# Performance work log

Hardware: AMD Instinct MI355X
Metric: run time of the kernel (lower is better)

## Reference

```python
import jax, jax.numpy as jnp
import numpy as np

B, S, K, D, H, F = 2, 2048, 2048, 1024, 16, 4096
HD = D // H
LN_EPS = 1e-5  # nn.LayerNorm default (module's eps arg is unused by the norms)


def setup_inputs() -> dict:
    key = jax.random.key(0)
    ks = jax.random.split(key, 12)
    def w(k, shape, scale=0.02):
        return jax.random.normal(k, shape, jnp.float32) * scale
    return {
        "x": jax.random.normal(ks[0], (B, S, D), jnp.float32),
        "context": jax.random.normal(ks[1], (B, K, D), jnp.float32),
        "Wq": w(ks[2], (D, D)), "bq": jnp.zeros((D,), jnp.float32),
        "Wk": w(ks[3], (D, D)), "bk": jnp.zeros((D,), jnp.float32),
        "Wv": w(ks[4], (D, D)), "bv": jnp.zeros((D,), jnp.float32),
        "W1": w(ks[5], (F, D)), "b1": jnp.zeros((F,), jnp.float32),
        "W2": w(ks[6], (D, F)), "b2": jnp.zeros((D,), jnp.float32),
        "g1": jnp.ones((D,), jnp.float32), "be1": jnp.zeros((D,), jnp.float32),
        "g2": jnp.ones((D,), jnp.float32), "be2": jnp.zeros((D,), jnp.float32),
    }


def _ln(x, g, b):
    m = jnp.mean(x, axis=-1, keepdims=True)
    v = jnp.var(x, axis=-1, keepdims=True)
    return (x - m) / jnp.sqrt(v + LN_EPS) * g + b


def _split_heads(t, L):
    # [B, L, D] -> [B, H, L, HD]
    return t.reshape(B, L, H, HD).transpose(0, 2, 1, 3)


def reference(x, context, Wq, bq, Wk, bk, Wv, bv, W1, b1, W2, b2, g1, be1, g2, be2):
    q = _split_heads(x @ Wq.T + bq, S)
    k = _split_heads(context @ Wk.T + bk, K)
    v = _split_heads(context @ Wv.T + bv, K)
    # NOTE: original scales by sqrt(encoder_out_dim), not sqrt(head_dim)
    scores = jnp.einsum('bhqd,bhkd->bhqk', q, k) / jnp.sqrt(jnp.float32(D))
    attn = jax.nn.softmax(scores, axis=-1)
    ctx = jnp.einsum('bhqk,bhkd->bhqd', attn, v)
    # faithful to original: raw reshape of [B,H,S,HD] -> [B,S,D] (no head transpose)
    out1 = ctx.reshape(B, S, D)
    out1 = x + _ln(out1, g1, be1)
    h = jax.nn.gelu(out1 @ W1.T + b1, approximate=False)
    out2 = _ln(h @ W2.T + b2, g2, be2)
    return out1 + out2
```

## Files before the change

### kernel.cpp

```cpp
#include <hip/hip_runtime.h>
#include <hip/hip_bf16.h>

#define BB 2
#define SS 2048
#define KK 2048
#define DD 1024
#define HH 16
#define FF 4096

using bf16x8 = __attribute__((ext_vector_type(8))) __bf16;
using f32x4  = __attribute__((ext_vector_type(4))) float;
using u16 = unsigned short;

__device__ __forceinline__ float bf2f(u16 u){
  union { unsigned int i; float f; } c; c.i = ((unsigned int)u) << 16; return c.f;
}
__device__ __forceinline__ u16 f2bf(float f){
  union { float f; unsigned int i; } c; c.f = f;
  return (u16)((c.i + 0x7fffu + ((c.i >> 16) & 1u)) >> 16);
}
__device__ __forceinline__ float gelu_exact(float x){
  return 0.5f * x * (1.f + erff(x * 0.70710678118654752f));
}

__device__ __forceinline__ void gll16(const void* g, const void* l) {
  __builtin_amdgcn_global_load_lds(
      (const __attribute__((address_space(1))) void*)(unsigned long long)(size_t)g,
      (__attribute__((address_space(3))) void*)(unsigned int)(size_t)l,
      16, 0, 0);
}

#define E_X   0
#define E_CX  4194304
#define E_WQ  8388608
#define E_BQ  9437184
#define E_WK  9438208
#define E_BK  10486784
#define E_WV  10487808
#define E_BV  11536384
#define E_W1  11537408
#define E_B1  15731712
#define E_W2  15735808
#define E_B2  19930112
#define E_G1  19931136
#define E_BE1 19932160
#define E_G2  19933184
#define E_BE2 19934208
#define E_TOT 19935232

struct Ptrs { const void* p[16]; };

__global__ __launch_bounds__(256)
void convert_inputs(Ptrs ptrs, u16* __restrict__ dst)
{
  const bool is_f32 = (((const u16*)ptrs.p[12])[0] == 0);
  const int szs[16] = {4194304, 4194304, 1048576, 1024, 1048576, 1024,
                       1048576, 1024, 4194304, 4096, 4194304, 1024,
                       1024, 1024, 1024, 1024};
  long long gbase = (long long)blockIdx.x * 1024;
  int seg = 0; long long start = 0;
  while (seg < 15 && gbase >= start + szs[seg]) { start += szs[seg]; seg++; }
  const long long local = gbase - start;
  const int tid = threadIdx.x;
  u16 outv[4];
  if (is_f32) {
    const float4* s = (const float4*)((const float*)ptrs.p[seg] + local);
    float4 v = s[tid];
    outv[0] = f2bf(v.x); outv[1] = f2bf(v.y); outv[2] = f2bf(v.z); outv[3] = f2bf(v.w);
  } else {
    const uint2* s = (const uint2*)((const u16*)ptrs.p[seg] + local);
    uint2 v = s[tid];
    *(uint2*)outv = v;
  }
  *(uint2*)(dst + gbase + (long long)tid * 4) = *(uint2*)outv;
}

template<int EPI>
__device__ __forceinline__
void gemm_core(const u16* __restrict__ A, const u16* __restrict__ W,
               const u16* __restrict__ bias, void* __restrict__ Cout,
               int N, int Kd, int lda, int n0, int m0,
               u16* sA0, u16* sA1, u16* sB0, u16* sB1)
{
  const int tid = threadIdx.x;
  const int wv = tid >> 6, lane = tid & 63;
  const int wm = (wv >> 1) * 64, wn = (wv & 1) * 64;
  const int l16 = lane & 15, quad = lane >> 4;
  const int srow = tid >> 2;
  const int scol = ((tid & 3) ^ ((srow >> 1) & 3)) * 8;

  const u16* gA = A + (size_t)(m0 + srow) * lda + scol;
  const u16* gB = W + (size_t)(n0 + srow) * lda + scol;
  u16* lA0 = sA0 + wv * 512; u16* lA1 = sA1 + wv * 512;
  u16* lB0 = sB0 + wv * 512; u16* lB1 = sB1 + wv * 512;
  const size_t rs = (size_t)64 * lda;

  f32x4 acc[4][4] = {};

  auto mma_step = [&](const u16* sA, const u16* sB) {
    bf16x8 af[4], wf[4];
#pragma unroll
    for (int i = 0; i < 4; i++) {
      const int row = wm + 16 * i + l16;
      af[i] = *(const bf16x8*)(sA + row * 32 + (quad ^ ((row >> 1) & 3)) * 8);
    }
#pragma unroll
    for (int j = 0; j < 4; j++) {
      const int row = wn + 16 * j + l16;
      wf[j] = *(const bf16x8*)(sB + row * 32 + (quad ^ ((row >> 1) & 3)) * 8);
    }
#pragma unroll
    for (int i = 0; i < 4; i++)
#pragma unroll
      for (int j = 0; j < 4; j++)
        acc[i][j] = __builtin_amdgcn_mfma_f32_16x16x32_bf16(af[i], wf[j], acc[i][j], 0, 0, 0);
  };

  gll16(gA, lA0); gll16(gA + rs, lA0 + 2048);
  gll16(gB, lB0); gll16(gB + rs, lB0 + 2048);

  for (int k0 = 0; k0 < Kd; k0 += 64) {
    __syncthreads();
    gll16(gA + k0 + 32, lA1); gll16(gA + rs + k0 + 32, lA1 + 2048);
    gll16(gB + k0 + 32, lB1); gll16(gB + rs + k0 + 32, lB1 + 2048);
    mma_step(sA0, sB0);
    __syncthreads();
    if (k0 + 64 < Kd) {
      gll16(gA + k0 + 64, lA0); gll16(gA + rs + k0 + 64, lA0 + 2048);
      gll16(gB + k0 + 64, lB0); gll16(gB + rs + k0 + 64, lB0 + 2048);
    }
    mma_step(sA1, sB1);
  }

#pragma unroll
  for (int i = 0; i < 4; i++)
#pragma unroll
    for (int j = 0; j < 4; j++) {
      const int mb = m0 + wm + 16 * i + quad * 4;
      const int n  = n0 + wn + 16 * j + l16;
      if (EPI == 4) {
#pragma unroll
        for (int r = 0; r < 4; r++)
          ((float*)Cout)[(size_t)(mb + r) * N + n] = acc[i][j][r];
      } else {
        const float bv = bf2f(bias[n]);
        if (EPI == 3) {
          u16 pk[4];
#pragma unroll
          for (int r = 0; r < 4; r++) pk[r] = f2bf(acc[i][j][r] + bv);
          const int b = mb >> 11, key = mb & 2047;
          *(uint2*)((u16*)Cout + ((size_t)((b * HH + (n >> 6)) * 64 + (n & 63))) * KK + key)
              = *(uint2*)pk;
        } else {
#pragma unroll
          for (int r = 0; r < 4; r++) {
            float vv = acc[i][j][r] + bv;
            if (EPI == 1) vv = gelu_exact(vv);
            ((u16*)Cout)[(size_t)(mb + r) * N + n] = f2bf(vv);
          }
        }
      }
    }
}

template<int EPI>
__global__ __launch_bounds__(256, 2)
void gemm_bt(const u16* __restrict__ A, const u16* __restrict__ W,
             const u16* __restrict__ bias, void* __restrict__ Cout,
             int N, int Kd, int lda)
{
  __shared__ u16 sA0[4096], sA1[4096], sB0[4096], sB1[4096];
  gemm_core<EPI>(A, W, bias, Cout, N, Kd, lda,
                 blockIdx.x * 128, blockIdx.y * 128, sA0, sA1, sB0, sB1);
}

__global__ __launch_bounds__(256, 2)
void qkv_gemm(const u16* __restrict__ conv, u16* __restrict__ q_ws,
              u16* __restrict__ k_ws, u16* __restrict__ vt_ws)
{
  __shared__ u16 sA0[4096], sA1[4096], sB0[4096], sB1[4096];
  const int n0 = blockIdx.x * 128, m0 = blockIdx.y * 128;
  const int z = blockIdx.z;
  if (z == 0)
    gemm_core<0>(conv + E_X,  conv + E_WQ, conv + E_BQ, q_ws,  DD, DD, DD, n0, m0, sA0, sA1, sB0, sB1);
  else if (z == 1)
    gemm_core<0>(conv + E_CX, conv + E_WK, conv + E_BK, k_ws,  DD, DD, DD, n0, m0, sA0, sA1, sB0, sB1);
  else
    gemm_core<3>(conv + E_CX, conv + E_WV, conv + E_BV, vt_ws, DD, DD, DD, n0, m0, sA0, sA1, sB0, sB1);
}

__global__ __launch_bounds__(256, 2)
void ffn2_gemm(const u16* __restrict__ h, const u16* __restrict__ W2,
               float* __restrict__ pa, float* __restrict__ pb)
{
  __shared__ u16 sA0[4096], sA1[4096], sB0[4096], sB1[4096];
  const int n0 = blockIdx.x * 128, m0 = blockIdx.y * 128;
  const int z = blockIdx.z;
  gemm_core<4>(h + z * 2048, W2 + z * 2048, nullptr, z ? pb : pa,
               DD, 2048, FF, n0, m0, sA0, sA1, sB0, sB1);
}

#define ATT_SCALE 0.03125f

__global__ __launch_bounds__(256, 2)
void attn_flash(const u16* __restrict__ q, const u16* __restrict__ k,
                const u16* __restrict__ vt, u16* __restrict__ ctx)
{
  __shared__ u16 Qs[128 * 64];
  __shared__ u16 Ks0[64 * 64], Ks1[64 * 64], Vt0[64 * 64], Vt1[64 * 64];
  __shared__ u16 Ps[4][32 * 72];
  const int tid = threadIdx.x, wv = tid >> 6, lane = tid & 63;
  const int l16 = lane & 15, quad = lane >> 4;
  const int s0 = blockIdx.x * 128;
  const int bh = blockIdx.y, b = bh >> 4, h = bh & 15;
  const size_t qgbase = ((size_t)b * SS + s0) * DD + h * 64;
  const size_t kgbase = (size_t)b * KK * DD + h * 64;
  const size_t vtbase = (size_t)bh * 64 * KK;
  const int srow = tid >> 3, sc8 = tid & 7;

  auto stage_kv = [&](u16* Ks, u16* Vt, int kt) {
#pragma unroll
    for (int n = 0; n < 2; n++) {
      int row = srow + 32 * n, c8 = sc8 ^ (row & 7);
      gll16(k + kgbase + (size_t)(kt + row) * DD + c8 * 8, Ks + (n * 256 + wv * 64) * 8);
      gll16(vt + vtbase + (size_t)row * KK + kt + c8 * 8, Vt + (n * 256 + wv * 64) * 8);
    }
  };

#pragma unroll
  for (int n = 0; n < 4; n++) {
    int row = srow + 32 * n, c8 = sc8 ^ (row & 7);
    gll16(q + qgbase + (size_t)row * DD + c8 * 8, Qs + (n * 256 + wv * 64) * 8);
  }
  stage_kv(Ks0, Vt0, 0);
  __syncthreads();

  bf16x8 qf[2][2];
#pragma unroll
  for (int mi = 0; mi < 2; mi++)
#pragma unroll
    for (int kc = 0; kc < 2; kc++)
      qf[mi][kc] = *(const bf16x8*)(Qs + (wv * 32 + mi * 16 + l16) * 64
                                    + (((kc << 2) | quad) ^ (l16 & 7)) * 8);

  f32x4 O[2][4] = {};
  float psum[2] = {0.f, 0.f};
  u16* Psw = Ps[wv];

  auto compute = [&](const u16* Ks, const u16* Vt) {
#pragma unroll
    for (int mi = 0; mi < 2; mi++) {
      uint2 pk2[4];
#pragma unroll
      for (int jj = 0; jj < 4; jj++) {
        f32x4 c = {};
#pragma unroll
        for (int kc = 0; kc < 2; kc++) {
          bf16x8 ak = *(const bf16x8*)(Ks + (jj * 16 + l16) * 64
                                       + (((kc << 2) | quad) ^ (l16 & 7)) * 8);
          c = __builtin_amdgcn_mfma_f32_16x16x32_bf16(ak, qf[mi][kc], c, 0, 0, 0);
        }
        float p0 = __expf(c[0] * ATT_SCALE);
        float p1 = __expf(c[1] * ATT_SCALE);
        float p2 = __expf(c[2] * ATT_SCALE);
        float p3 = __expf(c[3] * ATT_SCALE);
        psum[mi] += (p0 + p1) + (p2 + p3);
        union { float f; unsigned u; } u0{p0}, u1{p1}, u2{p2}, u3{p3};
        pk2[jj].x = __builtin_amdgcn_perm(u1.u, u0.u, 0x07060302u);
        pk2[jj].y = __builtin_amdgcn_perm(u3.u, u2.u, 0x07060302u);
      }
#pragma unroll
      for (int jj = 0; jj < 4; jj++)
        *(uint2*)(Psw + (mi * 16 + l16) * 72 + jj * 16 + quad * 4) = pk2[jj];
    }
    asm volatile("s_waitcnt lgkmcnt(0)" ::: "memory");
    bf16x8 pf[2][2];
#pragma unroll
    for (int mi = 0; mi < 2; mi++)
#pragma unroll
      for (int kc = 0; kc < 2; kc++)
        pf[mi][kc] = *(const bf16x8*)(Psw + (mi * 16 + l16) * 72 + kc * 32 + quad * 8);
#pragma unroll
    for (int mi = 0; mi < 2; mi++)
#pragma unroll
      for (int db = 0; db < 4; db++)
#pragma unroll
        for (int kc = 0; kc < 2; kc++) {
          bf16x8 bv = *(const bf16x8*)(Vt + (db * 16 + l16) * 64
                                       + (((kc << 2) | quad) ^ (l16 & 7)) * 8);
          O[mi][db] = __builtin_amdgcn_mfma_f32_16x16x32_bf16(pf[mi][kc], bv, O[mi][db], 0, 0, 0);
        }
  };

  for (int kt = 0; kt < KK; kt += 128) {
    __syncthreads();
    stage_kv(Ks1, Vt1, kt + 64);
    compute(Ks0, Vt0);
    __syncthreads();
    if (kt + 128 < KK) stage_kv(Ks0, Vt0, kt + 128);
    compute(Ks1, Vt1);
  }

  float lf[2];
#pragma unroll
  for (int mi = 0; mi < 2; mi++) {
    float t = psum[mi];
    t += __shfl_xor(t, 16, 64);
    t += __shfl_xor(t, 32, 64);
    lf[mi] = t;
  }
#pragma unroll
  for (int mi = 0; mi < 2; mi++)
#pragma unroll
    for (int r = 0; r < 4; r++) {
      float lv = __shfl(lf[mi], quad * 4 + r, 64);
      float inv = 1.f / lv;
      int qrow = s0 + wv * 32 + mi * 16 + quad * 4 + r;
#pragma unroll
      for (int db = 0; db < 4; db++)
        ctx[((size_t)bh * SS + qrow) * 64 + db * 16 + l16] = f2bf(O[mi][db][r] * inv);
    }
}

__global__ __launch_bounds__(256)
void ln1_res(const u16* __restrict__ src, const u16* __restrict__ x,
             const u16* __restrict__ g, const u16* __restrict__ be,
             u16* __restrict__ out_bf)
{
  const int row = blockIdx.x, tid = threadIdx.x;
  const size_t base = (size_t)row * 1024;
  float vv[4]; float s = 0.f, s2 = 0.f;
#pragma unroll
  for (int i = 0; i < 4; i++) {
    vv[i] = bf2f(src[base + tid + 256 * i]);
    s += vv[i]; s2 += vv[i] * vv[i];
  }
#pragma unroll
  for (int off = 32; off; off >>= 1) { s += __shfl_xor(s, off, 64); s2 += __shfl_xor(s2, off, 64); }
  __shared__ float red[2][4];
  const int wave = tid >> 6, lane = tid & 63;
  if (lane == 0) { red[0][wave] = s; red[1][wave] = s2; }
  __syncthreads();
  s  = red[0][0] + red[0][1] + red[0][2] + red[0][3];
  s2 = red[1][0] + red[1][1] + red[1][2] + red[1][3];
  const float mean = s * (1.f / 1024.f);
  const float rstd = rsqrtf(s2 * (1.f / 1024.f) - mean * mean + 1e-5f);
#pragma unroll
  for (int i = 0; i < 4; i++) {
    int col = tid + 256 * i;
    float nv = (vv[i] - mean) * rstd * bf2f(g[col]) + bf2f(be[col]);
    out_bf[base + col] = f2bf(bf2f(x[base + col]) + nv);
  }
}

__global__ __launch_bounds__(256)
void ln2_res(const float* __restrict__ pa, const float* __restrict__ pb,
             const u16* __restrict__ b2, const u16* __restrict__ o1,
             const u16* __restrict__ g, const u16* __restrict__ be,
             const void* __restrict__ detect, void* __restrict__ out)
{
  const bool f32out = (((const u16*)detect)[0] == 0);
  const int row = blockIdx.x, tid = threadIdx.x;
  const size_t base = (size_t)row * 1024;
  float vv[4]; float s = 0.f, s2 = 0.f;
#pragma unroll
  for (int i = 0; i < 4; i++) {
    int col = tid + 256 * i;
    vv[i] = pa[base + col] + pb[base + col] + bf2f(b2[col]);
    s += vv[i]; s2 += vv[i] * vv[i];
  }
#pragma unroll
  for (int off = 32; off; off >>= 1) { s += __shfl_xor(s, off, 64); s2 += __shfl_xor(s2, off, 64); }
  __shared__ float red[2][4];
  const int wave = tid >> 6, lane = tid & 63;
  if (lane == 0) { red[0][wave] = s; red[1][wave] = s2; }
  __syncthreads();
  s  = red[0][0] + red[0][1] + red[0][2] + red[0][3];
  s2 = red[1][0] + red[1][1] + red[1][2] + red[1][3];
  const float mean = s * (1.f / 1024.f);
  const float rstd = rsqrtf(s2 * (1.f / 1024.f) - mean * mean + 1e-5f);
#pragma unroll
  for (int i = 0; i < 4; i++) {
    int col = tid + 256 * i;
    float nv = (vv[i] - mean) * rstd * bf2f(g[col]) + bf2f(be[col]);
    float res = bf2f(o1[base + col]) + nv;
    if (f32out) ((float*)out)[base + col] = res;
    else        ((u16*)out)[base + col]  = f2bf(res);
  }
}

extern "C" void kernel_launch(void* const* d_in, const int* in_sizes, int n_in,
                              void* d_out, int out_size, void* d_ws, size_t ws_size,
                              hipStream_t stream)
{
  char* ws = (char*)d_ws;
  const size_t MB = 1024 * 1024;
  u16* conv   = (u16*)ws;
  u16* q_ws   = (u16*)(ws + 40 * MB);
  u16* k_ws   = (u16*)(ws + 48 * MB);
  u16* vt_ws  = (u16*)(ws + 56 * MB);
  u16* ctx_ws = (u16*)(ws + 64 * MB);
  u16* o1_bf  = (u16*)(ws + 72 * MB);
  u16* h_ws   = (u16*)(ws + 80 * MB);
  float* pa   = (float*)(ws + 40 * MB);
  float* pb   = (float*)(ws + 56 * MB);

  Ptrs ptrs;
  for (int i = 0; i < 16; i++) ptrs.p[i] = d_in[i];

  dim3 blk(256);
  const int M = BB * SS;

  convert_inputs<<<dim3(E_TOT / 1024), blk, 0, stream>>>(ptrs, conv);

  qkv_gemm<<<dim3(DD / 128, M / 128, 3), blk, 0, stream>>>(conv, q_ws, k_ws, vt_ws);

  attn_flash<<<dim3(SS / 128, BB * HH), blk, 0, stream>>>(q_ws, k_ws, vt_ws, ctx_ws);

  ln1_res<<<dim3(M), blk, 0, stream>>>(ctx_ws, conv + E_X, conv + E_G1, conv + E_BE1, o1_bf);

  gemm_bt<1><<<dim3(FF / 128, M / 128), blk, 0, stream>>>(o1_bf, conv + E_W1, conv + E_B1, h_ws, FF, DD, DD);

  ffn2_gemm<<<dim3(DD / 128, M / 128, 2), blk, 0, stream>>>(h_ws, conv + E_W2, pa, pb);

  ln2_res<<<dim3(M), blk, 0, stream>>>(pa, pb, conv + E_B2, o1_bf,
                                       conv + E_G2, conv + E_BE2, d_in[12], d_out);
}
```

Baseline: 344.1 us.

## Fuse LayerNorm1 and residual into attention epilogue; store FFN2 split-K partials as bf16

The attention kernel now applies LayerNorm1 and the residual add directly in its epilogue. It relies on the raw head reshape: each 16-query-row group of one head maps to exactly one 1024-wide output row, so a full-wave reduction gives the row statistics. This removes the ctx workspace round trip and the separate ln1_res launch. The FFN2 split-K partial sums are also written as bf16 instead of fp32, which halves that write and read traffic. The cost is some lost precision in the partials, plus strided, less coalesced output writes from the attention epilogue.

```diff
diff --git a/kernel.cpp b/kernel.cpp
--- a/kernel.cpp
+++ b/kernel.cpp
@@ -138,10 +138,10 @@
     for (int j = 0; j < 4; j++) {
       const int mb = m0 + wm + 16 * i + quad * 4;
       const int n  = n0 + wn + 16 * j + l16;
-      if (EPI == 4) {
+      if (EPI == 5) {
 #pragma unroll
         for (int r = 0; r < 4; r++)
-          ((float*)Cout)[(size_t)(mb + r) * N + n] = acc[i][j][r];
+          ((u16*)Cout)[(size_t)(mb + r) * N + n] = f2bf(acc[i][j][r]);
       } else {
         const float bv = bf2f(bias[n]);
         if (EPI == 3) {
@@ -191,12 +191,12 @@
 
 __global__ __launch_bounds__(256, 2)
 void ffn2_gemm(const u16* __restrict__ h, const u16* __restrict__ W2,
-               float* __restrict__ pa, float* __restrict__ pb)
+               u16* __restrict__ pa, u16* __restrict__ pb)
 {
   __shared__ u16 sA0[4096], sA1[4096], sB0[4096], sB1[4096];
   const int n0 = blockIdx.x * 128, m0 = blockIdx.y * 128;
   const int z = blockIdx.z;
-  gemm_core<4>(h + z * 2048, W2 + z * 2048, nullptr, z ? pb : pa,
+  gemm_core<5>(h + z * 2048, W2 + z * 2048, nullptr, z ? pb : pa,
                DD, 2048, FF, n0, m0, sA0, sA1, sB0, sB1);
 }
 
@@ -204,7 +204,9 @@
 
 __global__ __launch_bounds__(256, 2)
 void attn_flash(const u16* __restrict__ q, const u16* __restrict__ k,
-                const u16* __restrict__ vt, u16* __restrict__ ctx)
+                const u16* __restrict__ vt, const u16* __restrict__ x,
+                const u16* __restrict__ g1, const u16* __restrict__ be1,
+                u16* __restrict__ o1)
 {
   __shared__ u16 Qs[128 * 64];
   __shared__ u16 Ks0[64 * 64], Ks1[64 * 64], Vt0[64 * 64], Vt1[64 * 64];
@@ -309,30 +311,55 @@
     t += __shfl_xor(t, 32, 64);
     lf[mi] = t;
   }
-#pragma unroll
-  for (int mi = 0; mi < 2; mi++)
+
+#pragma unroll
+  for (int mi = 0; mi < 2; mi++) {
+    float v[4][4];
+    float s = 0.f, s2 = 0.f;
 #pragma unroll
     for (int r = 0; r < 4; r++) {
       float lv = __shfl(lf[mi], quad * 4 + r, 64);
       float inv = 1.f / lv;
-      int qrow = s0 + wv * 32 + mi * 16 + quad * 4 + r;
-#pragma unroll
-      for (int db = 0; db < 4; db++)
-        ctx[((size_t)bh * SS + qrow) * 64 + db * 16 + l16] = f2bf(O[mi][db][r] * inv);
-    }
+#pragma unroll
+      for (int db = 0; db < 4; db++) {
+        float t = O[mi][db][r] * inv;
+        v[db][r] = t;
+        s += t; s2 += t * t;
+      }
+    }
+#pragma unroll
+    for (int off = 1; off < 64; off <<= 1) {
+      s  += __shfl_xor(s,  off, 64);
+      s2 += __shfl_xor(s2, off, 64);
+    }
+    const float mean = s * (1.f / 1024.f);
+    const float rstd = rsqrtf(s2 * (1.f / 1024.f) - mean * mean + 1e-5f);
+    const size_t base = ((size_t)(b * 2048 + h * 128 + (s0 >> 4) + wv * 2 + mi)) << 10;
+#pragma unroll
+    for (int r = 0; r < 4; r++)
+#pragma unroll
+      for (int db = 0; db < 4; db++) {
+        const int col = (quad * 4 + r) * 64 + db * 16 + l16;
+        float nv = (v[db][r] - mean) * rstd * bf2f(g1[col]) + bf2f(be1[col]);
+        o1[base + col] = f2bf(bf2f(x[base + col]) + nv);
+      }
+  }
 }
 
 __global__ __launch_bounds__(256)
-void ln1_res(const u16* __restrict__ src, const u16* __restrict__ x,
+void ln2_res(const u16* __restrict__ pa, const u16* __restrict__ pb,
+             const u16* __restrict__ b2, const u16* __restrict__ o1,
              const u16* __restrict__ g, const u16* __restrict__ be,
-             u16* __restrict__ out_bf)
-{
+             const void* __restrict__ detect, void* __restrict__ out)
+{
+  const bool f32out = (((const u16*)detect)[0] == 0);
   const int row = blockIdx.x, tid = threadIdx.x;
   const size_t base = (size_t)row * 1024;
   float vv[4]; float s = 0.f, s2 = 0.f;
 #pragma unroll
   for (int i = 0; i < 4; i++) {
-    vv[i] = bf2f(src[base + tid + 256 * i]);
+    int col = tid + 256 * i;
+    vv[i] = bf2f(pa[base + col]) + bf2f(pb[base + col]) + bf2f(b2[col]);
     s += vv[i]; s2 += vv[i] * vv[i];
   }
 #pragma unroll
@@ -349,40 +376,6 @@
   for (int i = 0; i < 4; i++) {
     int col = tid + 256 * i;
     float nv = (vv[i] - mean) * rstd * bf2f(g[col]) + bf2f(be[col]);
-    out_bf[base + col] = f2bf(bf2f(x[base + col]) + nv);
-  }
-}
-
-__global__ __launch_bounds__(256)
-void ln2_res(const float* __restrict__ pa, const float* __restrict__ pb,
-             const u16* __restrict__ b2, const u16* __restrict__ o1,
-             const u16* __restrict__ g, const u16* __restrict__ be,
-             const void* __restrict__ detect, void* __restrict__ out)
-{
-  const bool f32out = (((const u16*)detect)[0] == 0);
-  const int row = blockIdx.x, tid = threadIdx.x;
-  const size_t base = (size_t)row * 1024;
-  float vv[4]; float s = 0.f, s2 = 0.f;
-#pragma unroll
-  for (int i = 0; i < 4; i++) {
-    int col = tid + 256 * i;
-    vv[i] = pa[base + col] + pb[base + col] + bf2f(b2[col]);
-    s += vv[i]; s2 += vv[i] * vv[i];
-  }
-#pragma unroll
-  for (int off = 32; off; off >>= 1) { s += __shfl_xor(s, off, 64); s2 += __shfl_xor(s2, off, 64); }
-  __shared__ float red[2][4];
-  const int wave = tid >> 6, lane = tid & 63;
-  if (lane == 0) { red[0][wave] = s; red[1][wave] = s2; }
-  __syncthreads();
-  s  = red[0][0] + red[0][1] + red[0][2] + red[0][3];
-  s2 = red[1][0] + red[1][1] + red[1][2] + red[1][3];
-  const float mean = s * (1.f / 1024.f);
-  const float rstd = rsqrtf(s2 * (1.f / 1024.f) - mean * mean + 1e-5f);
-#pragma unroll
-  for (int i = 0; i < 4; i++) {
-    int col = tid + 256 * i;
-    float nv = (vv[i] - mean) * rstd * bf2f(g[col]) + bf2f(be[col]);
     float res = bf2f(o1[base + col]) + nv;
     if (f32out) ((float*)out)[base + col] = res;
     else        ((u16*)out)[base + col]  = f2bf(res);
@@ -399,11 +392,10 @@
   u16* q_ws   = (u16*)(ws + 40 * MB);
   u16* k_ws   = (u16*)(ws + 48 * MB);
   u16* vt_ws  = (u16*)(ws + 56 * MB);
-  u16* ctx_ws = (u16*)(ws + 64 * MB);
-  u16* o1_bf  = (u16*)(ws + 72 * MB);
+  u16* o1_bf  = (u16*)(ws + 64 * MB);
   u16* h_ws   = (u16*)(ws + 80 * MB);
-  float* pa   = (float*)(ws + 40 * MB);
-  float* pb   = (float*)(ws + 56 * MB);
+  u16* pa     = q_ws;
+  u16* pb     = k_ws;
 
   Ptrs ptrs;
   for (int i = 0; i < 16; i++) ptrs.p[i] = d_in[i];
@@ -415,9 +407,8 @@
 
   qkv_gemm<<<dim3(DD / 128, M / 128, 3), blk, 0, stream>>>(conv, q_ws, k_ws, vt_ws);
 
-  attn_flash<<<dim3(SS / 128, BB * HH), blk, 0, stream>>>(q_ws, k_ws, vt_ws, ctx_ws);
-
-  ln1_res<<<dim3(M), blk, 0, stream>>>(ctx_ws, conv + E_X, conv + E_G1, conv + E_BE1, o1_bf);
+  attn_flash<<<dim3(SS / 128, BB * HH), blk, 0, stream>>>(
+      q_ws, k_ws, vt_ws, conv + E_X, conv + E_G1, conv + E_BE1, o1_bf);
 
   gemm_bt<1><<<dim3(FF / 128, M / 128), blk, 0, stream>>>(o1_bf, conv + E_W1, conv + E_B1, h_ws, FF, DD, DD);
 
```

Result: faster. 330.6 us (-3.9%).
